# Kernel optimization log

Measured on AMD Instinct MI355X. Metric: run time of the kernel, lower is better.

The kernel has to match this reference:

```python
import jax, jax.numpy as jnp
import numpy as np

N_NODES = 50000   # number of graph nodes
N_EDGES = 800000  # avg degree 16
D = 128           # in_dim == all hdims -> residual active every layer
L = 3             # len(cfg['hdims'])


def setup_inputs() -> dict:
    key = jax.random.key(0)
    ks = jax.random.split(key, 8)
    scale = 1.0 / np.sqrt(D)
    x = jax.random.normal(ks[0], (N_NODES, D), dtype=jnp.float32)
    edge_index = jax.random.randint(ks[1], (2, N_EDGES), 0, N_NODES, dtype=jnp.int32)
    in_fc_w = jax.random.normal(ks[2], (D, D), dtype=jnp.float32) * scale
    in_fc_b = jnp.zeros((D,), dtype=jnp.float32)
    # GraphConv per layer: lin_rel (with bias) applied to aggregated neighbors,
    # lin_root (no bias) applied to self features. All layers are DxD -> stack.
    w_rel = jax.random.normal(ks[3], (L, D, D), dtype=jnp.float32) * scale
    b_rel = jnp.zeros((L, D), dtype=jnp.float32)
    w_root = jax.random.normal(ks[4], (L, D, D), dtype=jnp.float32) * scale
    return {"x": x, "edge_index": edge_index, "in_fc_w": in_fc_w,
            "in_fc_b": in_fc_b, "w_rel": w_rel, "b_rel": b_rel, "w_root": w_root}


def reference(x, edge_index, in_fc_w, in_fc_b, w_rel, b_rel, w_root):
    src, dst = edge_index[0], edge_index[1]
    h = x @ in_fc_w + in_fc_b                     # in_fc
    for l in range(L):                            # fixed small layer count
        # GraphConv, aggr='add': gather source feats, scatter-add to targets
        agg = jax.ops.segment_sum(h[src], dst, num_segments=N_NODES)  # [N, D]
        out = agg @ w_rel[l] + b_rel[l] + h @ w_root[l]
        out = jax.nn.relu(out)
        h = out + h                               # residual (dims match)
    return h
```

## Files before the change

### kernel.cpp

```cpp
#include <hip/hip_runtime.h>
#include <hip/hip_bf16.h>


constexpr int D = 128;
constexpr int NB_SHIFT = 7;
constexpr int BCAP = 2560;
constexpr int STRIDE = 3456;
constexpr int CHUNK = 2048;

typedef __attribute__((ext_vector_type(8))) short bf16x8;
typedef __attribute__((ext_vector_type(4))) float f32x4;
typedef __attribute__((ext_vector_type(4))) unsigned int u32x4;

__device__ inline unsigned short f2bf(float f) {
    unsigned int u = __builtin_bit_cast(unsigned int, f);
    u += 0x7FFFu + ((u >> 16) & 1u);
    return (unsigned short)(u >> 16);
}
__device__ inline float bf2f(unsigned short v) {
    return __builtin_bit_cast(float, (unsigned int)v << 16);
}
__device__ inline float bf2f_lo(unsigned int v) {
    return __builtin_bit_cast(float, v << 16);
}
__device__ inline float bf2f_hi(unsigned int v) {
    return __builtin_bit_cast(float, v & 0xFFFF0000u);
}

__global__ __launch_bounds__(256) void prep(
    const float* __restrict__ x, const float* __restrict__ fc_w,
    const float* __restrict__ w_rel, const float* __restrict__ w_root,
    unsigned short* __restrict__ xb, unsigned short* __restrict__ Wp,
    int* __restrict__ cursor, unsigned short* __restrict__ hb0,
    unsigned short* __restrict__ hb1, int n4, int NB, int N)
{
    int blk = blockIdx.x;
    const int nconv = (n4 + 255) / 256;
    if (blk < nconv) {
        int i = blk * 256 + threadIdx.x;
        if (i < n4) {
            float4 v = ((const float4*)x)[i];
            ushort4 o;
            o.x = f2bf(v.x); o.y = f2bf(v.y); o.z = f2bf(v.z); o.w = f2bf(v.w);
            ((ushort4*)xb)[i] = o;
        }
        return;
    }
    blk -= nconv;
    if (blk < 56) {
        int idx = blk * 256 + threadIdx.x;
        int mat  = idx >> 11;
        int rem  = idx & 2047;
        int tn   = rem >> 8;
        int ks   = (rem >> 6) & 3;
        int lane = rem & 63;
        const float* w = (mat == 0) ? fc_w
                       : (mat <= 3) ? w_rel  + (size_t)(mat - 1) * D * D
                                    : w_root + (size_t)(mat - 4) * D * D;
        unsigned short* wp = Wp + (size_t)mat * D * D + (size_t)rem * 8;
        int kbase = ks * 32 + (lane >> 4) * 8;
        int col   = tn * 16 + (lane & 15);
        #pragma unroll
        for (int j = 0; j < 8; ++j)
            wp[j] = f2bf(w[(size_t)(kbase + j) * D + col]);
        return;
    }
    blk -= 56;
    const int ncb = (NB + 255) / 256;
    if (blk < ncb) {
        int i = blk * 256 + threadIdx.x;
        if (i < NB) cursor[i] = 0;
        return;
    }
    if (threadIdx.x < 64)
        ((unsigned int*)(hb0 + (size_t)N * D))[threadIdx.x] = 0u;
    else if (threadIdx.x < 128)
        ((unsigned int*)(hb1 + (size_t)N * D))[threadIdx.x - 64] = 0u;
}

__global__ __launch_bounds__(256) void gemm_mfma(
    const unsigned short* __restrict__ A1, const unsigned short* __restrict__ W1p,
    const float* __restrict__ bias, unsigned short* __restrict__ hb_out, int N)
{
    const int tid  = threadIdx.x;
    const int wave = tid >> 6;
    const int lane = tid & 63;
    const int row0 = blockIdx.x * 64 + wave * 16;
    const int mrow = lane & 15;
    const int kgrp = lane >> 4;

    f32x4 acc[8];
    #pragma unroll
    for (int t = 0; t < 8; ++t) acc[t] = (f32x4){0.f, 0.f, 0.f, 0.f};

    int arow = row0 + mrow; if (arow >= N) arow = N - 1;
    const size_t abase = (size_t)arow * D + kgrp * 8;

    #pragma unroll
    for (int ks = 0; ks < 4; ++ks) {
        bf16x8 a1 = *(const bf16x8*)(A1 + abase + ks * 32);
        #pragma unroll
        for (int tn = 0; tn < 8; ++tn) {
            bf16x8 b = *(const bf16x8*)(W1p + ((size_t)((tn * 4 + ks) * 64 + lane) * 8));
            acc[tn] = __builtin_amdgcn_mfma_f32_16x16x32_bf16(a1, b, acc[tn], 0, 0, 0);
        }
    }

    const int r0 = row0 + kgrp * 4;
    #pragma unroll
    for (int tn = 0; tn < 8; ++tn) {
        const int col = tn * 16 + mrow;
        const float bv = bias[col];
        #pragma unroll
        for (int reg = 0; reg < 4; ++reg) {
            int r = r0 + reg;
            if (r < N) hb_out[(size_t)r * D + col] = f2bf(acc[tn][reg] + bv);
        }
    }
}

__global__ __launch_bounds__(256) void layer_fused(
    const unsigned short* __restrict__ hb_in, const int* __restrict__ eb,
    const unsigned int* __restrict__ sorted_off,
    const unsigned short* __restrict__ Wrel, const unsigned short* __restrict__ Wroot,
    const float* __restrict__ bias,
    unsigned short* hb_out, float* out_f32, int N)
{
    __shared__ unsigned short aggt[16][136];

    const int tid   = threadIdx.x;
    const int wave  = tid >> 6;
    const int lane  = tid & 63;
    const int node0 = blockIdx.x * 16;

    {
        const int g = lane >> 4;
        const int c = lane & 15;
        const int n = node0 + wave * 4 + g;

        float acc[8];
        #pragma unroll
        for (int q = 0; q < 8; ++q) acc[q] = 0.f;

        if (n < N) {
            const int2 be = ((const int2*)eb)[n];
            int j = be.x;
            const int e = be.y;
            const unsigned int c16 = (unsigned int)c * 16u;
            const char* hb = (const char*)hb_in;
            if (j < e) {
                u32x4 iA = *(const u32x4*)(sorted_off + j);
                u32x4 iB = *(const u32x4*)(sorted_off + j + 4);
                for (;;) {
                    u32x4 v0 = *(const u32x4*)(hb + (iA[0] + c16));
                    u32x4 v1 = *(const u32x4*)(hb + (iA[1] + c16));
                    u32x4 v2 = *(const u32x4*)(hb + (iA[2] + c16));
                    u32x4 v3 = *(const u32x4*)(hb + (iA[3] + c16));
                    u32x4 v4 = *(const u32x4*)(hb + (iB[0] + c16));
                    u32x4 v5 = *(const u32x4*)(hb + (iB[1] + c16));
                    u32x4 v6 = *(const u32x4*)(hb + (iB[2] + c16));
                    u32x4 v7 = *(const u32x4*)(hb + (iB[3] + c16));
                    const bool more = (j + 8 < e);
                    u32x4 nA, nB;
                    if (more) {
                        nA = *(const u32x4*)(sorted_off + j + 8);
                        nB = *(const u32x4*)(sorted_off + j + 12);
                    }
                    #pragma unroll
                    for (int q = 0; q < 4; ++q) {
                        acc[2 * q]     += ((bf2f_lo(v0[q]) + bf2f_lo(v1[q])) + (bf2f_lo(v2[q]) + bf2f_lo(v3[q])))
                                        + ((bf2f_lo(v4[q]) + bf2f_lo(v5[q])) + (bf2f_lo(v6[q]) + bf2f_lo(v7[q])));
                        acc[2 * q + 1] += ((bf2f_hi(v0[q]) + bf2f_hi(v1[q])) + (bf2f_hi(v2[q]) + bf2f_hi(v3[q])))
                                        + ((bf2f_hi(v4[q]) + bf2f_hi(v5[q])) + (bf2f_hi(v6[q]) + bf2f_hi(v7[q])));
                    }
                    if (!more) break;
                    iA = nA; iB = nB; j += 8;
                }
            }
        }
        u32x4 o;
        #pragma unroll
        for (int q = 0; q < 4; ++q)
            o[q] = (unsigned int)f2bf(acc[2 * q]) |
                   ((unsigned int)f2bf(acc[2 * q + 1]) << 16);
        *(u32x4*)&aggt[wave * 4 + g][c * 8] = o;
    }
    __syncthreads();

    const int mrow = lane & 15;
    const int kgrp = lane >> 4;

    f32x4 acc2[2];
    acc2[0] = (f32x4){0.f, 0.f, 0.f, 0.f};
    acc2[1] = (f32x4){0.f, 0.f, 0.f, 0.f};

    int arow = node0 + mrow; if (arow >= N) arow = N - 1;
    const size_t abase = (size_t)arow * D + kgrp * 8;

    #pragma unroll
    for (int ks = 0; ks < 4; ++ks) {
        bf16x8 a1 = *(const bf16x8*)&aggt[mrow][ks * 32 + kgrp * 8];
        bf16x8 a2 = *(const bf16x8*)(hb_in + abase + ks * 32);
        #pragma unroll
        for (int t = 0; t < 2; ++t) {
            const int tn = wave * 2 + t;
            bf16x8 b1 = *(const bf16x8*)(Wrel  + ((size_t)((tn * 4 + ks) * 64 + lane) * 8));
            acc2[t] = __builtin_amdgcn_mfma_f32_16x16x32_bf16(a1, b1, acc2[t], 0, 0, 0);
            bf16x8 b2 = *(const bf16x8*)(Wroot + ((size_t)((tn * 4 + ks) * 64 + lane) * 8));
            acc2[t] = __builtin_amdgcn_mfma_f32_16x16x32_bf16(a2, b2, acc2[t], 0, 0, 0);
        }
    }

    const int r0 = node0 + kgrp * 4;
    #pragma unroll
    for (int t = 0; t < 2; ++t) {
        const int tn  = wave * 2 + t;
        const int col = tn * 16 + mrow;
        const float bv = bias[col];
        #pragma unroll
        for (int reg = 0; reg < 4; ++reg) {
            int r = r0 + reg;
            if (r < N) {
                float z = fmaxf(acc2[t][reg] + bv, 0.f);
                float o = z + bf2f(hb_in[(size_t)r * D + col]);
                if (out_f32 != nullptr) out_f32[(size_t)r * D + col] = o;
                else                    hb_out[(size_t)r * D + col] = f2bf(o);
            }
        }
    }
}

__global__ __launch_bounds__(256) void bucket_scatter(
    const int* __restrict__ src, const int* __restrict__ dst,
    unsigned int* __restrict__ entries, int* __restrict__ cursor, int E, int NB)
{
    __shared__ unsigned int   stage[CHUNK];
    __shared__ unsigned short bslot[CHUNK];
    __shared__ int lhist[512];
    __shared__ int lscan[512];
    __shared__ int lgbase[512];
    __shared__ int lcur[512];
    __shared__ int sh[256];

    const int base  = blockIdx.x * CHUNK;
    const int count = min(CHUNK, E - base);
    const int tid   = threadIdx.x;

    for (int i = tid; i < 512; i += 256) { lhist[i] = 0; lcur[i] = 0; }
    __syncthreads();

    for (int i = tid; i < count; i += 256)
        atomicAdd(&lhist[dst[base + i] >> NB_SHIFT], 1);
    __syncthreads();

    int v2 = lhist[2 * tid] + lhist[2 * tid + 1];
    sh[tid] = v2;
    __syncthreads();
    #pragma unroll
    for (int off = 1; off < 256; off <<= 1) {
        int t = (tid >= off) ? sh[tid - off] : 0;
        __syncthreads();
        sh[tid] += t;
        __syncthreads();
    }
    int excl2 = sh[tid] - v2;
    lscan[2 * tid]     = excl2;
    lscan[2 * tid + 1] = excl2 + lhist[2 * tid];
    __syncthreads();

    for (int t = tid; t < 512; t += 256) {
        int c = (t < NB) ? lhist[t] : 0;
        lgbase[t] = (c > 0) ? atomicAdd(&cursor[t], c) : 0;
    }
    __syncthreads();

    for (int i = tid; i < count; i += 256) {
        int d = dst[base + i];
        int s = src[base + i];
        int b = d >> NB_SHIFT;
        int p = atomicAdd(&lcur[b], 1);
        int slot = lscan[b] + p;
        stage[slot] = ((unsigned int)(d & ((1 << NB_SHIFT) - 1)) << 16) | (unsigned int)s;
        bslot[slot] = (unsigned short)b;
    }
    __syncthreads();

    for (int i = tid; i < count; i += 256) {
        int b   = bslot[i];
        int off = i - lscan[b] + lgbase[b];
        if (off < BCAP) entries[(size_t)b * BCAP + off] = stage[i];
    }
}

__global__ __launch_bounds__(256) void bucket_sort(
    const unsigned int* __restrict__ entries, const int* __restrict__ cursor,
    unsigned int* __restrict__ sorted_off, int* __restrict__ eb,
    int N, int NB, float inv_range, unsigned int zero_off)
{
    const int b   = blockIdx.x;
    const int tid = threadIdx.x;

    __shared__ int nhist[512];
    __shared__ int nscan[512];
    __shared__ int ncur[512];
    __shared__ int nbase[129];
    __shared__ int sh[256];
    __shared__ unsigned int svals[STRIDE];

    const int cnt = min(cursor[b], BCAP);

    for (int i = tid; i < 512; i += 256) { nhist[i] = 0; ncur[i] = 0; }
    __syncthreads();

    const unsigned int* ebase = entries + (size_t)b * BCAP;
    for (int i = tid; i < cnt; i += 256) {
        unsigned int e = ebase[i];
        int s = (int)(e & 0xFFFFu);
        int r = (int)((float)s * inv_range); if (r > 3) r = 3;
        atomicAdd(&nhist[(int)((e >> 16) << 2) | r], 1);
    }
    __syncthreads();

    int c4 = 0, pc = 0;
    if (tid < 128) {
        c4 = nhist[4 * tid] + nhist[4 * tid + 1] + nhist[4 * tid + 2] + nhist[4 * tid + 3];
        pc = (c4 + 7) & ~7;
    }
    sh[tid] = (tid < 128) ? pc : 0;
    __syncthreads();
    #pragma unroll
    for (int off = 1; off < 128; off <<= 1) {
        int t = (tid >= off && tid < 128) ? sh[tid - off] : 0;
        __syncthreads();
        if (tid < 128) sh[tid] += t;
        __syncthreads();
    }
    if (tid < 128) nbase[tid] = sh[tid] - pc;
    if (tid == 127) nbase[128] = sh[127];
    __syncthreads();
    const int padded_total = nbase[128];

    if (tid < 128) {
        int base = nbase[tid];
        int a0 = nhist[4 * tid], a1 = nhist[4 * tid + 1], a2 = nhist[4 * tid + 2];
        nscan[4 * tid]     = base;
        nscan[4 * tid + 1] = base + a0;
        nscan[4 * tid + 2] = base + a0 + a1;
        nscan[4 * tid + 3] = base + a0 + a1 + a2;
        int nn = (b << NB_SHIFT) + tid;
        if (nn < N) {
            eb[2 * nn]     = b * STRIDE + base;
            eb[2 * nn + 1] = b * STRIDE + base + pc;
        }
    }
    for (int i = tid; i < padded_total; i += 256) svals[i] = zero_off;
    __syncthreads();

    for (int i = tid; i < cnt; i += 256) {
        unsigned int e = ebase[i];
        int s = (int)(e & 0xFFFFu);
        int r = (int)((float)s * inv_range); if (r > 3) r = 3;
        int key = (int)((e >> 16) << 2) | r;
        int p = atomicAdd(&ncur[key], 1);
        svals[nscan[key] + p] = ((unsigned int)s) << 8;
    }
    __syncthreads();

    unsigned int* obase = sorted_off + (size_t)b * STRIDE;
    for (int i = tid; i < padded_total; i += 256) obase[i] = svals[i];
}

extern "C" void kernel_launch(void* const* d_in, const int* in_sizes, int n_in,
                              void* d_out, int out_size, void* d_ws, size_t ws_size,
                              hipStream_t stream)
{
    const float* x      = (const float*)d_in[0];
    const int*   ei     = (const int*)  d_in[1];
    const float* fc_w   = (const float*)d_in[2];
    const float* fc_b   = (const float*)d_in[3];
    const float* w_rel  = (const float*)d_in[4];
    const float* b_rel  = (const float*)d_in[5];
    const float* w_root = (const float*)d_in[6];
    float* out = (float*)d_out;

    const int N = in_sizes[0] / D;
    const int E = in_sizes[1] / 2;
    const int* src = ei;
    const int* dst = ei + E;
    const int NB = (N + (1 << NB_SHIFT) - 1) >> NB_SHIFT;

    char* p = (char*)d_ws;
    unsigned short* hb0 = (unsigned short*)p;  p += (size_t)(N + 1) * D * sizeof(unsigned short);
    unsigned short* hb1 = (unsigned short*)p;  p += (size_t)(N + 1) * D * sizeof(unsigned short);
    unsigned short* Wp  = (unsigned short*)p;  p += (size_t)7 * D * D * sizeof(unsigned short);
    unsigned int* sorted_off = (unsigned int*)p;  p += (size_t)NB * STRIDE * sizeof(unsigned int);
    int* eb     = (int*)p;                     p += (size_t)2 * N * sizeof(int);
    int* cursor = (int*)p;                     p += (size_t)NB * sizeof(int);
    unsigned int* entries = (unsigned int*)d_out;

    unsigned short* Wp_in   = Wp;
    unsigned short* Wp_rel  = Wp + (size_t)1 * D * D;
    unsigned short* Wp_root = Wp + (size_t)4 * D * D;
    unsigned short* xb = hb1;

    const int n4 = N * D / 4;
    const int gemm_blocks  = (N + 63) / 64;
    const int layer_blocks = (N + 15) / 16;
    const int prep_blocks  = (n4 + 255) / 256 + 56 + (NB + 255) / 256 + 1;

    prep<<<prep_blocks, 256, 0, stream>>>(x, fc_w, w_rel, w_root, xb, Wp, cursor,
                                          hb0, hb1, n4, NB, N);

    bucket_scatter<<<(E + CHUNK - 1) / CHUNK, 256, 0, stream>>>(
        src, dst, entries, cursor, E, NB);
    bucket_sort<<<NB, 256, 0, stream>>>(
        entries, cursor, sorted_off, eb, N, NB, 4.0f / (float)N,
        ((unsigned int)N) << 8);

    gemm_mfma<<<gemm_blocks, 256, 0, stream>>>(xb, Wp_in, fc_b, hb0, N);

    unsigned short* hin  = hb0;
    unsigned short* hout = hb1;
    for (int l = 0; l < 3; ++l) {
        layer_fused<<<layer_blocks, 256, 0, stream>>>(
            hin, eb, sorted_off,
            Wp_rel + (size_t)l * D * D, Wp_root + (size_t)l * D * D,
            b_rel + (size_t)l * D,
            (l == 2) ? nullptr : hout,
            (l == 2) ? out : nullptr, N);
        unsigned short* t = hin; hin = hout; hout = t;
    }
}
```

Before: 239.2 us.

## Replace two-level bucket sort CSR build with per-node count/scan/atomic scatter

Replaces the shared-memory bucketed scatter and per-bucket sort with three simpler kernels: a global per-node degree count via atomics, a per-128-node block scan that writes padded offsets and zero-fill padding, and a direct atomic scatter of source indices into per-node slots. This removes the staging buffer and the sub-range ordering of sources inside each node's list, trading shared-memory work for many global atomics. Neighbor order within a node becomes nondeterministic and no longer grouped by source range, which may hurt gather locality in the layer kernels. It also drops the BCAP overflow clamp, so a bucket whose padded total exceeds STRIDE could now write past its region.

New measurement: 301.3 us. +25.9%, slower.

```diff
diff --git a/kernel.cpp b/kernel.cpp
--- a/kernel.cpp
+++ b/kernel.cpp
@@ -4,9 +4,7 @@
 
 constexpr int D = 128;
 constexpr int NB_SHIFT = 7;
-constexpr int BCAP = 2560;
 constexpr int STRIDE = 3456;
-constexpr int CHUNK = 2048;
 
 typedef __attribute__((ext_vector_type(8))) short bf16x8;
 typedef __attribute__((ext_vector_type(4))) float f32x4;
@@ -31,8 +29,8 @@
     const float* __restrict__ x, const float* __restrict__ fc_w,
     const float* __restrict__ w_rel, const float* __restrict__ w_root,
     unsigned short* __restrict__ xb, unsigned short* __restrict__ Wp,
-    int* __restrict__ cursor, unsigned short* __restrict__ hb0,
-    unsigned short* __restrict__ hb1, int n4, int NB, int N)
+    int* __restrict__ deg, unsigned short* __restrict__ hb0,
+    unsigned short* __restrict__ hb1, int n4, int N)
 {
     int blk = blockIdx.x;
     const int nconv = (n4 + 255) / 256;
@@ -66,16 +64,79 @@
         return;
     }
     blk -= 56;
-    const int ncb = (NB + 255) / 256;
-    if (blk < ncb) {
+    const int ndb = (N + 255) / 256;
+    if (blk < ndb) {
         int i = blk * 256 + threadIdx.x;
-        if (i < NB) cursor[i] = 0;
+        if (i < N) deg[i] = 0;
         return;
     }
     if (threadIdx.x < 64)
         ((unsigned int*)(hb0 + (size_t)N * D))[threadIdx.x] = 0u;
     else if (threadIdx.x < 128)
         ((unsigned int*)(hb1 + (size_t)N * D))[threadIdx.x - 64] = 0u;
+}
+
+__global__ __launch_bounds__(256) void edge_count(
+    const int* __restrict__ dst, int* __restrict__ deg, int E)
+{
+    int i = blockIdx.x * 256 + threadIdx.x;
+    int e4 = E >> 2;
+    if (i < e4) {
+        int4 d = ((const int4*)dst)[i];
+        atomicAdd(&deg[d.x], 1);
+        atomicAdd(&deg[d.y], 1);
+        atomicAdd(&deg[d.z], 1);
+        atomicAdd(&deg[d.w], 1);
+    }
+    if (i == 0) {
+        for (int j = e4 << 2; j < E; ++j) atomicAdd(&deg[dst[j]], 1);
+    }
+}
+
+__global__ __launch_bounds__(128) void node_scan(
+    int* __restrict__ deg, int* __restrict__ eb,
+    unsigned int* __restrict__ sorted_off, int N, unsigned int zero_off)
+{
+    const int b   = blockIdx.x;
+    const int tid = threadIdx.x;
+    const int n   = (b << NB_SHIFT) + tid;
+
+    __shared__ int sh[128];
+
+    int d  = (n < N) ? deg[n] : 0;
+    int pc = (d + 7) & ~7;
+    sh[tid] = pc;
+    __syncthreads();
+    #pragma unroll
+    for (int off = 1; off < 128; off <<= 1) {
+        int t = (tid >= off) ? sh[tid - off] : 0;
+        __syncthreads();
+        sh[tid] += t;
+        __syncthreads();
+    }
+    const int base = sh[tid] - pc;
+
+    if (n < N) {
+        eb[2 * n]     = b * STRIDE + base;
+        eb[2 * n + 1] = b * STRIDE + base + pc;
+        deg[n] = 0;
+        unsigned int* so = sorted_off + (size_t)b * STRIDE + base;
+        for (int k = d; k < pc; ++k) so[k] = zero_off;
+    }
+}
+
+__global__ __launch_bounds__(256) void edge_scatter(
+    const int* __restrict__ src, const int* __restrict__ dst,
+    const int* __restrict__ eb, int* __restrict__ cur,
+    unsigned int* __restrict__ sorted_off, int E)
+{
+    int i = blockIdx.x * 256 + threadIdx.x;
+    if (i < E) {
+        int s = src[i];
+        int d = dst[i];
+        int p = atomicAdd(&cur[d], 1);
+        sorted_off[eb[2 * d] + p] = ((unsigned int)s) << 8;
+    }
 }
 
 __global__ __launch_bounds__(256) void gemm_mfma(
@@ -230,146 +291,6 @@
     }
 }
 
-__global__ __launch_bounds__(256) void bucket_scatter(
-    const int* __restrict__ src, const int* __restrict__ dst,
-    unsigned int* __restrict__ entries, int* __restrict__ cursor, int E, int NB)
-{
-    __shared__ unsigned int   stage[CHUNK];
-    __shared__ unsigned short bslot[CHUNK];
-    __shared__ int lhist[512];
-    __shared__ int lscan[512];
-    __shared__ int lgbase[512];
-    __shared__ int lcur[512];
-    __shared__ int sh[256];
-
-    const int base  = blockIdx.x * CHUNK;
-    const int count = min(CHUNK, E - base);
-    const int tid   = threadIdx.x;
-
-    for (int i = tid; i < 512; i += 256) { lhist[i] = 0; lcur[i] = 0; }
-    __syncthreads();
-
-    for (int i = tid; i < count; i += 256)
-        atomicAdd(&lhist[dst[base + i] >> NB_SHIFT], 1);
-    __syncthreads();
-
-    int v2 = lhist[2 * tid] + lhist[2 * tid + 1];
-    sh[tid] = v2;
-    __syncthreads();
-    #pragma unroll
-    for (int off = 1; off < 256; off <<= 1) {
-        int t = (tid >= off) ? sh[tid - off] : 0;
-        __syncthreads();
-        sh[tid] += t;
-        __syncthreads();
-    }
-    int excl2 = sh[tid] - v2;
-    lscan[2 * tid]     = excl2;
-    lscan[2 * tid + 1] = excl2 + lhist[2 * tid];
-    __syncthreads();
-
-    for (int t = tid; t < 512; t += 256) {
-        int c = (t < NB) ? lhist[t] : 0;
-        lgbase[t] = (c > 0) ? atomicAdd(&cursor[t], c) : 0;
-    }
-    __syncthreads();
-
-    for (int i = tid; i < count; i += 256) {
-        int d = dst[base + i];
-        int s = src[base + i];
-        int b = d >> NB_SHIFT;
-        int p = atomicAdd(&lcur[b], 1);
-        int slot = lscan[b] + p;
-        stage[slot] = ((unsigned int)(d & ((1 << NB_SHIFT) - 1)) << 16) | (unsigned int)s;
-        bslot[slot] = (unsigned short)b;
-    }
-    __syncthreads();
-
-    for (int i = tid; i < count; i += 256) {
-        int b   = bslot[i];
-        int off = i - lscan[b] + lgbase[b];
-        if (off < BCAP) entries[(size_t)b * BCAP + off] = stage[i];
-    }
-}
-
-__global__ __launch_bounds__(256) void bucket_sort(
-    const unsigned int* __restrict__ entries, const int* __restrict__ cursor,
-    unsigned int* __restrict__ sorted_off, int* __restrict__ eb,
-    int N, int NB, float inv_range, unsigned int zero_off)
-{
-    const int b   = blockIdx.x;
-    const int tid = threadIdx.x;
-
-    __shared__ int nhist[512];
-    __shared__ int nscan[512];
-    __shared__ int ncur[512];
-    __shared__ int nbase[129];
-    __shared__ int sh[256];
-    __shared__ unsigned int svals[STRIDE];
-
-    const int cnt = min(cursor[b], BCAP);
-
-    for (int i = tid; i < 512; i += 256) { nhist[i] = 0; ncur[i] = 0; }
-    __syncthreads();
-
-    const unsigned int* ebase = entries + (size_t)b * BCAP;
-    for (int i = tid; i < cnt; i += 256) {
-        unsigned int e = ebase[i];
-        int s = (int)(e & 0xFFFFu);
-        int r = (int)((float)s * inv_range); if (r > 3) r = 3;
-        atomicAdd(&nhist[(int)((e >> 16) << 2) | r], 1);
-    }
-    __syncthreads();
-
-    int c4 = 0, pc = 0;
-    if (tid < 128) {
-        c4 = nhist[4 * tid] + nhist[4 * tid + 1] + nhist[4 * tid + 2] + nhist[4 * tid + 3];
-        pc = (c4 + 7) & ~7;
-    }
-    sh[tid] = (tid < 128) ? pc : 0;
-    __syncthreads();
-    #pragma unroll
-    for (int off = 1; off < 128; off <<= 1) {
-        int t = (tid >= off && tid < 128) ? sh[tid - off] : 0;
-        __syncthreads();
-        if (tid < 128) sh[tid] += t;
-        __syncthreads();
-    }
-    if (tid < 128) nbase[tid] = sh[tid] - pc;
-    if (tid == 127) nbase[128] = sh[127];
-    __syncthreads();
-    const int padded_total = nbase[128];
-
-    if (tid < 128) {
-        int base = nbase[tid];
-        int a0 = nhist[4 * tid], a1 = nhist[4 * tid + 1], a2 = nhist[4 * tid + 2];
-        nscan[4 * tid]     = base;
-        nscan[4 * tid + 1] = base + a0;
-        nscan[4 * tid + 2] = base + a0 + a1;
-        nscan[4 * tid + 3] = base + a0 + a1 + a2;
-        int nn = (b << NB_SHIFT) + tid;
-        if (nn < N) {
-            eb[2 * nn]     = b * STRIDE + base;
-            eb[2 * nn + 1] = b * STRIDE + base + pc;
-        }
-    }
-    for (int i = tid; i < padded_total; i += 256) svals[i] = zero_off;
-    __syncthreads();
-
-    for (int i = tid; i < cnt; i += 256) {
-        unsigned int e = ebase[i];
-        int s = (int)(e & 0xFFFFu);
-        int r = (int)((float)s * inv_range); if (r > 3) r = 3;
-        int key = (int)((e >> 16) << 2) | r;
-        int p = atomicAdd(&ncur[key], 1);
-        svals[nscan[key] + p] = ((unsigned int)s) << 8;
-    }
-    __syncthreads();
-
-    unsigned int* obase = sorted_off + (size_t)b * STRIDE;
-    for (int i = tid; i < padded_total; i += 256) obase[i] = svals[i];
-}
-
 extern "C" void kernel_launch(void* const* d_in, const int* in_sizes, int n_in,
                               void* d_out, int out_size, void* d_ws, size_t ws_size,
                               hipStream_t stream)
@@ -394,9 +315,8 @@
     unsigned short* hb1 = (unsigned short*)p;  p += (size_t)(N + 1) * D * sizeof(unsigned short);
     unsigned short* Wp  = (unsigned short*)p;  p += (size_t)7 * D * D * sizeof(unsigned short);
     unsigned int* sorted_off = (unsigned int*)p;  p += (size_t)NB * STRIDE * sizeof(unsigned int);
-    int* eb     = (int*)p;                     p += (size_t)2 * N * sizeof(int);
-    int* cursor = (int*)p;                     p += (size_t)NB * sizeof(int);
-    unsigned int* entries = (unsigned int*)d_out;
+    int* eb  = (int*)p;                        p += (size_t)2 * N * sizeof(int);
+    int* deg = (int*)p;                        p += (size_t)N * sizeof(int);
 
     unsigned short* Wp_in   = Wp;
     unsigned short* Wp_rel  = Wp + (size_t)1 * D * D;
@@ -406,16 +326,15 @@
     const int n4 = N * D / 4;
     const int gemm_blocks  = (N + 63) / 64;
     const int layer_blocks = (N + 15) / 16;
-    const int prep_blocks  = (n4 + 255) / 256 + 56 + (NB + 255) / 256 + 1;
-
-    prep<<<prep_blocks, 256, 0, stream>>>(x, fc_w, w_rel, w_root, xb, Wp, cursor,
-                                          hb0, hb1, n4, NB, N);
-
-    bucket_scatter<<<(E + CHUNK - 1) / CHUNK, 256, 0, stream>>>(
-        src, dst, entries, cursor, E, NB);
-    bucket_sort<<<NB, 256, 0, stream>>>(
-        entries, cursor, sorted_off, eb, N, NB, 4.0f / (float)N,
-        ((unsigned int)N) << 8);
+    const int prep_blocks  = (n4 + 255) / 256 + 56 + (N + 255) / 256 + 1;
+    const unsigned int zero_off = ((unsigned int)N) << 8;
+
+    prep<<<prep_blocks, 256, 0, stream>>>(x, fc_w, w_rel, w_root, xb, Wp, deg,
+                                          hb0, hb1, n4, N);
+
+    edge_count<<<(E / 4 + 255) / 256, 256, 0, stream>>>(dst, deg, E);
+    node_scan<<<NB, 128, 0, stream>>>(deg, eb, sorted_off, N, zero_off);
+    edge_scatter<<<(E + 255) / 256, 256, 0, stream>>>(src, dst, eb, deg, sorted_off, E);
 
     gemm_mfma<<<gemm_blocks, 256, 0, stream>>>(xb, Wp_in, fc_b, hb0, N);
 
```
